# Kernel tuning notes

Hardware: AMD Instinct MI355X
Metric: run time of the kernel (lower is better)

Reference implementation:

```python
import jax, jax.numpy as jnp
import numpy as np


def setup_inputs() -> dict:
    key = jax.random.key(0)
    k1, k2, k3, k4 = jax.random.split(key, 4)
    B, S, IN, OUT, ORG = 8, 4096, 1536, 3072, 4
    fan_in_std = (1.0 / IN) ** 0.5
    x = jax.random.normal(k1, (B, S, IN), dtype=jnp.float32)
    weight = jax.random.normal(k2, (ORG, IN, OUT), dtype=jnp.float32) * fan_in_std
    bias = jax.random.normal(k3, (ORG, OUT), dtype=jnp.float32) * 0.01
    organism_index = jax.random.randint(k4, (B,), 0, ORG, dtype=jnp.int64)
    return {"x": x, "organism_index": organism_index, "weight": weight, "bias": bias}


def reference(x, organism_index, weight, bias):
    # Gather per-sample weight [B, IN, OUT] and bias [B, OUT]
    w = weight[organism_index].astype(x.dtype)          # [B, IN, OUT]
    b = bias[organism_index].astype(x.dtype)            # [B, OUT]
    # x: [B, S, IN] -> [B, S, OUT]; bias broadcast over inner dims
    out = jnp.einsum('bsi,bij->bsj', x, w) + b[:, None, :]
    return out
```

## Files before the change

kernel.cpp:

```cpp
#include <hip/hip_runtime.h>
#include <hip/hip_bf16.h>
#include <stdint.h>

typedef __attribute__((ext_vector_type(4))) float f32x4;
typedef __attribute__((ext_vector_type(8))) short short8;

#define DIM_S 4096
#define DIM_IN 1536
#define DIM_OUT 3072
#define NB 8
#define NORG 4

#define XB_ELEMS (NB * DIM_S * DIM_IN)
#define WT_ELEMS (NORG * DIM_OUT * DIM_IN)
#define WS_NEED ((size_t)(XB_ELEMS + WT_ELEMS) * 2)

__device__ __forceinline__ unsigned short f2bf(float f) {
    union { __hip_bfloat16 h; unsigned short u; } c;
    c.h = __float2bfloat16(f);
    return c.u;
}

__device__ __forceinline__ void gload16(const void* g, void* l) {
    __builtin_amdgcn_global_load_lds(
        (const __attribute__((address_space(1))) unsigned int*)g,
        (__attribute__((address_space(3))) unsigned int*)l, 16, 0, 0);
}

__global__ __launch_bounds__(256) void cvt_x(const float* __restrict__ x,
                                             unsigned short* __restrict__ xb) {
    const int nchunk = XB_ELEMS / 8;
    for (int c = blockIdx.x * 256 + threadIdx.x; c < nchunk; c += gridDim.x * 256) {
        const float4 v0 = *reinterpret_cast<const float4*>(x + (size_t)c * 8);
        const float4 v1 = *reinterpret_cast<const float4*>(x + (size_t)c * 8 + 4);
        union { unsigned short u[8]; short8 v; } p;
        p.u[0] = f2bf(v0.x); p.u[1] = f2bf(v0.y); p.u[2] = f2bf(v0.z); p.u[3] = f2bf(v0.w);
        p.u[4] = f2bf(v1.x); p.u[5] = f2bf(v1.y); p.u[6] = f2bf(v1.z); p.u[7] = f2bf(v1.w);
        *reinterpret_cast<short8*>(xb + (size_t)c * 8) = p.v;
    }
}

__global__ __launch_bounds__(256) void cvt_wt(const float* __restrict__ w,
                                              unsigned short* __restrict__ wt) {
    __shared__ unsigned short T[64][68];
    const int bid = blockIdx.x;
    const int org = bid / (24 * 48);
    const int rem = bid % (24 * 48);
    const int k0 = (rem / 48) * 64;
    const int n0 = (rem % 48) * 64;
    const float* __restrict__ wp = w + (size_t)org * DIM_IN * DIM_OUT;
    unsigned short* __restrict__ op = wt + (size_t)org * DIM_OUT * DIM_IN;
    const int t = threadIdx.x;
    #pragma unroll
    for (int i = 0; i < 4; ++i) {
        const int c = t + 256 * i;
        const int kk = c >> 4, nq = (c & 15) * 4;
        const float4 v = *reinterpret_cast<const float4*>(
            wp + (size_t)(k0 + kk) * DIM_OUT + n0 + nq);
        ushort4 pv;
        pv.x = f2bf(v.x); pv.y = f2bf(v.y); pv.z = f2bf(v.z); pv.w = f2bf(v.w);
        *reinterpret_cast<ushort4*>(&T[kk][nq]) = pv;
    }
    __syncthreads();
    #pragma unroll
    for (int i = 0; i < 2; ++i) {
        const int c = t + 256 * i;
        const int n = c >> 3, k8 = (c & 7) * 8;
        union { unsigned short u[8]; short8 v; } p;
        #pragma unroll
        for (int j = 0; j < 8; ++j) p.u[j] = T[k8 + j][n];
        *reinterpret_cast<short8*>(op + (size_t)(n0 + n) * DIM_IN + k0 + k8) = p.v;
    }
}

__global__ __launch_bounds__(512, 2) void mol_gemm_8p(
    const unsigned short* __restrict__ xb, const int* __restrict__ orgidx,
    const unsigned short* __restrict__ wt, const float* __restrict__ bias,
    float* __restrict__ out)
{
    __shared__ __align__(16) unsigned short LDS[2][4][8192];

    const int tid  = threadIdx.x;
    const int lane = tid & 63;
    const int wave = tid >> 6;
    const int wr = wave >> 2;
    const int wc = wave & 3;
    const int l15 = lane & 15;
    const int q16 = lane >> 4;

    const int bid = blockIdx.x;
    const int id  = (bid & 7) * 192 + (bid >> 3);
    const int row0 = (id / 12) * 256;
    const int col0 = (id % 12) * 256;
    const int batch = row0 >> 12;
    const int org   = orgidx[batch];

    const unsigned short* __restrict__ Abase = xb + (size_t)row0 * DIM_IN;
    const unsigned short* __restrict__ Bbase =
        wt + (size_t)org * DIM_OUT * DIM_IN + (size_t)col0 * DIM_IN;

    const int rA = tid >> 2;
    const int qs = ((tid & 3) ^ (((tid >> 5) & 1) << 1)) * 8;
    const unsigned short* pA0 = Abase + (size_t)rA * DIM_IN + qs;
    const unsigned short* pA1 = Abase + (size_t)(128 + rA) * DIM_IN + qs;
    const unsigned short* pB0 = Bbase + (size_t)rA * DIM_IN + qs;
    const unsigned short* pB1 = Bbase + (size_t)(128 + rA) * DIM_IN + qs;

    const int d0 = wave * 512;
    const int d1 = 4096 + wave * 512;

    const int swb = ((l15 >> 3) & 1) << 1;
    const int offA0 = ((wr * 128 + l15) * 32 + ((q16 ^ swb) << 3)) * 2;
    const int offB0 = ((wc * 64  + l15) * 32 + ((q16 ^ swb) << 3)) * 2;

    f32x4 acc[8][4] = {};
    short8 af4[4], bfr[4];

#define STG(buf, slot, p0, p1, kofs) do {                      \
        gload16((p0) + (kofs), &LDS[buf][slot][d0]);           \
        gload16((p1) + (kofs), &LDS[buf][slot][d1]);           \
    } while (0)

#define RD_A4(buf, kk, mih) do {                                            \
        const char* bA_ = (const char*)(&LDS[buf][kk][0]) + offA0           \
                          + 4096 * (mih);                                   \
        _Pragma("unroll")                                                   \
        for (int i_ = 0; i_ < 4; ++i_)                                      \
            af4[i_] = *reinterpret_cast<const short8*>(bA_ + 1024 * i_);    \
    } while (0)

#define RD_B4(buf, kk) do {                                                 \
        const char* bB_ = (const char*)(&LDS[buf][2 + (kk)][0]) + offB0;    \
        _Pragma("unroll")                                                   \
        for (int i_ = 0; i_ < 4; ++i_)                                      \
            bfr[i_] = *reinterpret_cast<const short8*>(bB_ + 1024 * i_);    \
    } while (0)

#define MM(mih) do {                                                        \
        __builtin_amdgcn_s_setprio(1);                                      \
        _Pragma("unroll")                                                   \
        for (int i_ = 0; i_ < 4; ++i_) {                                    \
            _Pragma("unroll")                                               \
            for (int n_ = 0; n_ < 4; ++n_)                                  \
                acc[(mih)*4 + i_][n_] =                                     \
                    __builtin_amdgcn_mfma_f32_16x16x32_bf16(                \
                        af4[i_], bfr[n_], acc[(mih)*4 + i_][n_], 0, 0, 0);  \
        }                                                                   \
        __builtin_amdgcn_s_setprio(0);                                      \
    } while (0)

#define BAR  do { __builtin_amdgcn_s_barrier();                             \
                  asm volatile("" ::: "memory"); } while (0)
#define SB0  __builtin_amdgcn_sched_barrier(0)
#define WAIT8 asm volatile("s_waitcnt vmcnt(8)" ::: "memory")

    STG(0, 0, pA0, pA1, 0);
    STG(0, 2, pB0, pB1, 0);
    STG(0, 1, pA0, pA1, 32);
    STG(0, 3, pB0, pB1, 32);
    STG(1, 0, pA0, pA1, 64);
    STG(1, 2, pB0, pB1, 64);
    WAIT8;
    BAR;

    int kA = 96, kB = 96;

#define PHASE(buf, kk, mih, sbuf, sslot, pp0, pp1, kref, wait8) do {        \
        RD_A4(buf, kk, mih);                                                \
        if ((mih) == 0) RD_B4(buf, kk);                                     \
        STG(sbuf, sslot, pp0, pp1, kref);                                   \
        if (kref < 1504) kref += 32;                                        \
        BAR; SB0;                                                           \
        MM(mih);                                                            \
        if (wait8) WAIT8;                                                   \
        BAR;                                                                \
    } while (0)

#define TILE(buf, obuf) do {                                                \
        PHASE(buf, 0, 0, obuf, 1, pA0, pA1, kA, 0);                         \
        PHASE(buf, 0, 1, obuf, 3, pB0, pB1, kB, 1);                         \
        PHASE(buf, 1, 0, buf,  0, pA0, pA1, kA, 0);                         \
        PHASE(buf, 1, 1, buf,  2, pB0, pB1, kB, 1);                         \
    } while (0)

    #pragma unroll 1
    for (int i = 0; i < 12; ++i) {
        TILE(0, 1);
        TILE(1, 0);
    }

    const float* __restrict__ bptr = bias + (size_t)org * DIM_OUT;
    const int crow = q16 * 4;
    const int ccol = l15;
    #pragma unroll
    for (int ni = 0; ni < 4; ++ni) {
        const int gc = col0 + wc * 64 + ni * 16 + ccol;
        const float bv = bptr[gc];
        #pragma unroll
        for (int mi = 0; mi < 8; ++mi) {
            const int gr = row0 + wr * 128 + mi * 16 + crow;
            #pragma unroll
            for (int r = 0; r < 4; ++r)
                out[(size_t)(gr + r) * DIM_OUT + gc] = acc[mi][ni][r] + bv;
        }
    }
#undef STG
#undef RD_A4
#undef RD_B4
#undef MM
#undef BAR
#undef SB0
#undef WAIT8
#undef PHASE
#undef TILE
}

#define BM 128
#define BN 128
#define BK 32
#define LDK 40
union BF8 { unsigned short u[8]; short8 v; };

__global__ __launch_bounds__(256) void mol_gemm_fb(
    const float* __restrict__ x, const int* __restrict__ orgidx,
    const float* __restrict__ weight, const float* __restrict__ bias,
    float* __restrict__ out)
{
    __shared__ __align__(16) unsigned short Alds[2][BM][LDK];
    __shared__ __align__(16) unsigned short Blds[2][BN][LDK];

    const int tid  = threadIdx.x;
    const int lane = tid & 63;
    const int wave = tid >> 6;
    const int wr = wave >> 1, wc = wave & 1;

    const int bid = blockIdx.x;
    const int id  = (bid & 7) * 768 + (bid >> 3);
    const int row0 = (id / 24) * BM;
    const int col0 = (id % 24) * BN;

    const int batch = row0 / DIM_S;
    const int org   = orgidx[batch];
    const float* __restrict__ W = weight + (size_t)org * DIM_IN * DIM_OUT;

    f32x4 acc[4][4] = {};
    const int ar  = tid >> 2;
    const int ak8 = (tid & 3) * 8;
    const int bn  = tid & 127;
    const int bg0 = tid >> 7;
    const float* __restrict__ xbase = x + (size_t)row0 * DIM_IN;
    const float* __restrict__ wbase = W + col0 + bn;

    auto stage = [&](int buf, int k0) {
        #pragma unroll
        for (int i = 0; i < 2; ++i) {
            const int r = ar + 64 * i;
            const float* xp = xbase + (size_t)r * DIM_IN + k0 + ak8;
            const float4 v0 = *reinterpret_cast<const float4*>(xp);
            const float4 v1 = *reinterpret_cast<const float4*>(xp + 4);
            BF8 p;
            p.u[0] = f2bf(v0.x); p.u[1] = f2bf(v0.y);
            p.u[2] = f2bf(v0.z); p.u[3] = f2bf(v0.w);
            p.u[4] = f2bf(v1.x); p.u[5] = f2bf(v1.y);
            p.u[6] = f2bf(v1.z); p.u[7] = f2bf(v1.w);
            *reinterpret_cast<short8*>(&Alds[buf][r][ak8]) = p.v;
        }
        #pragma unroll
        for (int j = 0; j < 2; ++j) {
            const int g = bg0 + 2 * j;
            const float* wp = wbase + (size_t)(k0 + 8 * g) * DIM_OUT;
            BF8 p;
            #pragma unroll
            for (int r = 0; r < 8; ++r) p.u[r] = f2bf(wp[(size_t)r * DIM_OUT]);
            *reinterpret_cast<short8*>(&Blds[buf][bn][8 * g]) = p.v;
        }
    };

    stage(0, 0);
    const int nk = DIM_IN / BK;
    const int kq = (lane >> 4) * 8;
    const int lr = lane & 15;

    for (int t = 0; t < nk; ++t) {
        __syncthreads();
        const int cur = t & 1;
        if (t + 1 < nk) stage(cur ^ 1, (t + 1) * BK);
        short8 a[4], b[4];
        #pragma unroll
        for (int mi = 0; mi < 4; ++mi)
            a[mi] = *reinterpret_cast<const short8*>(&Alds[cur][wr * 64 + mi * 16 + lr][kq]);
        #pragma unroll
        for (int ni = 0; ni < 4; ++ni)
            b[ni] = *reinterpret_cast<const short8*>(&Blds[cur][wc * 64 + ni * 16 + lr][kq]);
        #pragma unroll
        for (int mi = 0; mi < 4; ++mi)
            #pragma unroll
            for (int ni = 0; ni < 4; ++ni)
                acc[mi][ni] = __builtin_amdgcn_mfma_f32_16x16x32_bf16(
                    a[mi], b[ni], acc[mi][ni], 0, 0, 0);
    }

    const float* __restrict__ bptr = bias + (size_t)org * DIM_OUT;
    const int crow = (lane >> 4) * 4;
    const int ccol = lane & 15;
    #pragma unroll
    for (int ni = 0; ni < 4; ++ni) {
        const int gc = col0 + wc * 64 + ni * 16 + ccol;
        const float bv = bptr[gc];
        #pragma unroll
        for (int mi = 0; mi < 4; ++mi) {
            const int gr = row0 + wr * 64 + mi * 16 + crow;
            #pragma unroll
            for (int r = 0; r < 4; ++r)
                out[(size_t)(gr + r) * DIM_OUT + gc] = acc[mi][ni][r] + bv;
        }
    }
}

extern "C" void kernel_launch(void* const* d_in, const int* in_sizes, int n_in,
                              void* d_out, int out_size, void* d_ws, size_t ws_size,
                              hipStream_t stream)
{
    const float* x      = (const float*)d_in[0];
    const int*   orgidx = (const int*)d_in[1];
    const float* weight = (const float*)d_in[2];
    const float* bias   = (const float*)d_in[3];
    float* out = (float*)d_out;

    if (ws_size >= WS_NEED) {
        unsigned short* xbp = (unsigned short*)d_ws;
        unsigned short* wtp = xbp + XB_ELEMS;
        cvt_x<<<dim3(2048), dim3(256), 0, stream>>>(x, xbp);
        cvt_wt<<<dim3(NORG * 24 * 48), dim3(256), 0, stream>>>(weight, wtp);
        mol_gemm_8p<<<dim3(1536), dim3(512), 0, stream>>>(xbp, orgidx, wtp, bias, out);
    } else {
        mol_gemm_fb<<<dim3(6144), dim3(256), 0, stream>>>(x, orgidx, weight, bias, out);
    }
}
```

Measured before the change: 435.3 us.

## Double-buffer MFMA register fragments to overlap LDS reads with matrix math

Restructures the main GEMM loop so A/B fragments are read from LDS into a second register set while MFMAs run on the first, and removes the sched_barrier and one of the two barriers per phase. The waitcnt is changed from vmcnt(8) to vmcnt(4) to match the new staging order. The aim is to hide LDS read latency behind matrix work and cut synchronisation. In exchange it uses more VGPRs and relies on a delicate buffer-slot ordering, so any race or occupancy loss could offset the gain.

Result: no change. 429.0 us (-1.4%).

```diff
diff --git a/kernel.cpp b/kernel.cpp
--- a/kernel.cpp
+++ b/kernel.cpp
@@ -114,29 +114,29 @@
     const int offB0 = ((wc * 64  + l15) * 32 + ((q16 ^ swb) << 3)) * 2;
 
     f32x4 acc[8][4] = {};
-    short8 af4[4], bfr[4];
+    short8 af[2][4], bfr[2][4];
 
 #define STG(buf, slot, p0, p1, kofs) do {                      \
         gload16((p0) + (kofs), &LDS[buf][slot][d0]);           \
         gload16((p1) + (kofs), &LDS[buf][slot][d1]);           \
     } while (0)
 
-#define RD_A4(buf, kk, mih) do {                                            \
-        const char* bA_ = (const char*)(&LDS[buf][kk][0]) + offA0           \
+#define RD_A4(dst, buf, kk, mih) do {                                       \
+        const char* pA_ = (const char*)(&LDS[buf][kk][0]) + offA0           \
                           + 4096 * (mih);                                   \
         _Pragma("unroll")                                                   \
         for (int i_ = 0; i_ < 4; ++i_)                                      \
-            af4[i_] = *reinterpret_cast<const short8*>(bA_ + 1024 * i_);    \
+            af[dst][i_] = *reinterpret_cast<const short8*>(pA_ + 1024*i_);  \
     } while (0)
 
-#define RD_B4(buf, kk) do {                                                 \
-        const char* bB_ = (const char*)(&LDS[buf][2 + (kk)][0]) + offB0;    \
+#define RD_B4(dst, buf, kk) do {                                            \
+        const char* pB_ = (const char*)(&LDS[buf][2 + (kk)][0]) + offB0;    \
         _Pragma("unroll")                                                   \
         for (int i_ = 0; i_ < 4; ++i_)                                      \
-            bfr[i_] = *reinterpret_cast<const short8*>(bB_ + 1024 * i_);    \
+            bfr[dst][i_] = *reinterpret_cast<const short8*>(pB_ + 1024*i_); \
     } while (0)
 
-#define MM(mih) do {                                                        \
+#define MM(ca, cb, mih) do {                                                \
         __builtin_amdgcn_s_setprio(1);                                      \
         _Pragma("unroll")                                                   \
         for (int i_ = 0; i_ < 4; ++i_) {                                    \
@@ -144,15 +144,17 @@
             for (int n_ = 0; n_ < 4; ++n_)                                  \
                 acc[(mih)*4 + i_][n_] =                                     \
                     __builtin_amdgcn_mfma_f32_16x16x32_bf16(                \
-                        af4[i_], bfr[n_], acc[(mih)*4 + i_][n_], 0, 0, 0);  \
+                        af[ca][i_], bfr[cb][n_],                            \
+                        acc[(mih)*4 + i_][n_], 0, 0, 0);                    \
         }                                                                   \
         __builtin_amdgcn_s_setprio(0);                                      \
     } while (0)
 
 #define BAR  do { __builtin_amdgcn_s_barrier();                             \
                   asm volatile("" ::: "memory"); } while (0)
-#define SB0  __builtin_amdgcn_sched_barrier(0)
+#define WAIT4 asm volatile("s_waitcnt vmcnt(4)" ::: "memory")
 #define WAIT8 asm volatile("s_waitcnt vmcnt(8)" ::: "memory")
+#define KADV(k) do { if ((k) < 1504) (k) += 32; } while (0)
 
     STG(0, 0, pA0, pA1, 0);
     STG(0, 2, pB0, pB1, 0);
@@ -162,31 +164,33 @@
     STG(1, 2, pB0, pB1, 64);
     WAIT8;
     BAR;
+    RD_A4(0, 0, 0, 0);
+    RD_B4(0, 0, 0);
 
     int kA = 96, kB = 96;
 
-#define PHASE(buf, kk, mih, sbuf, sslot, pp0, pp1, kref, wait8) do {        \
-        RD_A4(buf, kk, mih);                                                \
-        if ((mih) == 0) RD_B4(buf, kk);                                     \
-        STG(sbuf, sslot, pp0, pp1, kref);                                   \
-        if (kref < 1504) kref += 32;                                        \
-        BAR; SB0;                                                           \
-        MM(mih);                                                            \
-        if (wait8) WAIT8;                                                   \
-        BAR;                                                                \
-    } while (0)
-
-#define TILE(buf, obuf) do {                                                \
-        PHASE(buf, 0, 0, obuf, 1, pA0, pA1, kA, 0);                         \
-        PHASE(buf, 0, 1, obuf, 3, pB0, pB1, kB, 1);                         \
-        PHASE(buf, 1, 0, buf,  0, pA0, pA1, kA, 0);                         \
-        PHASE(buf, 1, 1, buf,  2, pB0, pB1, kB, 1);                         \
-    } while (0)
+#define TILE2() do {                                                        \
+   STG(1,1,pA0,pA1,kA); KADV(kA); RD_A4(1, 0,0,1);                    \
+         MM(0,0,0);                 BAR;                                    \
+   STG(1,3,pB0,pB1,kB); KADV(kB); RD_A4(0, 0,1,0); RD_B4(1, 0,1);    \
+         MM(1,0,1);          WAIT4; BAR;                                    \
+   STG(0,0,pA0,pA1,kA); KADV(kA); RD_A4(1, 0,1,1);                    \
+         MM(0,1,0);                 BAR;                                    \
+   STG(0,2,pB0,pB1,kB); KADV(kB); RD_A4(0, 1,0,0); RD_B4(0, 1,0);    \
+         MM(1,1,1);          WAIT4; BAR;                                    \
+   STG(0,1,pA0,pA1,kA); KADV(kA); RD_A4(1, 1,0,1);                    \
+         MM(0,0,0);                 BAR;                                    \
+   STG(0,3,pB0,pB1,kB); KADV(kB); RD_A4(0, 1,1,0); RD_B4(1, 1,1);    \
+         MM(1,0,1);          WAIT4; BAR;                                    \
+   STG(1,0,pA0,pA1,kA); KADV(kA); RD_A4(1, 1,1,1);                    \
+         MM(0,1,0);                 BAR;                                    \
+   STG(1,2,pB0,pB1,kB); KADV(kB); RD_A4(0, 0,0,0); RD_B4(0, 0,0);    \
+         MM(1,1,1);          WAIT4; BAR;                                    \
+} while (0)
 
     #pragma unroll 1
     for (int i = 0; i < 12; ++i) {
-        TILE(0, 1);
-        TILE(1, 0);
+        TILE2();
     }
 
     const float* __restrict__ bptr = bias + (size_t)org * DIM_OUT;
@@ -209,10 +213,10 @@
 #undef RD_B4
 #undef MM
 #undef BAR
-#undef SB0
+#undef WAIT4
 #undef WAIT8
-#undef PHASE
-#undef TILE
+#undef KADV
+#undef TILE2
 }
 
 #define BM 128
```

## Replace 8-wave 256x256 GEMM with 4-wave 256x128 triple-buffered pipeline

Applied to the files above, without the earlier changes.

The main GEMM kernel moves from 512 threads on 256x256 tiles with a double-buffered two-half phase schedule to 256 threads on 256x128 tiles. It uses a three-stage LDS ring with one barrier per K-step, and global loads for the next stage are issued between the MFMA halves. This is meant to cut barrier count and improve latency hiding while keeping two blocks per CU. In exchange, the smaller N tile means A is reloaded twice as often, so global and L2 traffic per FLOP goes up, and the grid doubles to 3072 blocks.

After: 455.5 us. +4.6%, slower.

```diff
diff --git a/kernel.cpp b/kernel.cpp
--- a/kernel.cpp
+++ b/kernel.cpp
@@ -73,27 +73,26 @@
     }
 }
 
-__global__ __launch_bounds__(512, 2) void mol_gemm_8p(
+__global__ __launch_bounds__(256, 2) void mol_gemm_3b(
     const unsigned short* __restrict__ xb, const int* __restrict__ orgidx,
     const unsigned short* __restrict__ wt, const float* __restrict__ bias,
     float* __restrict__ out)
 {
-    __shared__ __align__(16) unsigned short LDS[2][4][8192];
+    __shared__ __align__(16) unsigned short LDS[3][12288];
 
     const int tid  = threadIdx.x;
     const int lane = tid & 63;
     const int wave = tid >> 6;
-    const int wr = wave >> 2;
-    const int wc = wave & 3;
+    const int wr = wave >> 1;
+    const int wc = wave & 1;
     const int l15 = lane & 15;
     const int q16 = lane >> 4;
 
     const int bid = blockIdx.x;
-    const int id  = (bid & 7) * 192 + (bid >> 3);
-    const int row0 = (id / 12) * 256;
-    const int col0 = (id % 12) * 256;
-    const int batch = row0 >> 12;
-    const int org   = orgidx[batch];
+    const int id  = (bid & 7) * 384 + (bid >> 3);
+    const int row0 = (id / 24) * 256;
+    const int col0 = (id % 24) * 128;
+    const int org  = orgidx[row0 >> 12];
 
     const unsigned short* __restrict__ Abase = xb + (size_t)row0 * DIM_IN;
     const unsigned short* __restrict__ Bbase =
@@ -101,39 +100,45 @@
 
     const int rA = tid >> 2;
     const int qs = ((tid & 3) ^ (((tid >> 5) & 1) << 1)) * 8;
-    const unsigned short* pA0 = Abase + (size_t)rA * DIM_IN + qs;
-    const unsigned short* pA1 = Abase + (size_t)(128 + rA) * DIM_IN + qs;
-    const unsigned short* pB0 = Bbase + (size_t)rA * DIM_IN + qs;
-    const unsigned short* pB1 = Bbase + (size_t)(128 + rA) * DIM_IN + qs;
-
-    const int d0 = wave * 512;
-    const int d1 = 4096 + wave * 512;
+    const unsigned short* pa0 = Abase + (size_t)(rA      ) * DIM_IN + qs;
+    const unsigned short* pa1 = Abase + (size_t)(rA +  64) * DIM_IN + qs;
+    const unsigned short* pa2 = Abase + (size_t)(rA + 128) * DIM_IN + qs;
+    const unsigned short* pa3 = Abase + (size_t)(rA + 192) * DIM_IN + qs;
+    const unsigned short* pb0 = Bbase + (size_t)(rA      ) * DIM_IN + qs;
+    const unsigned short* pb1 = Bbase + (size_t)(rA +  64) * DIM_IN + qs;
 
     const int swb = ((l15 >> 3) & 1) << 1;
-    const int offA0 = ((wr * 128 + l15) * 32 + ((q16 ^ swb) << 3)) * 2;
-    const int offB0 = ((wc * 64  + l15) * 32 + ((q16 ^ swb) << 3)) * 2;
+    const int lof = l15 * 64 + ((q16 ^ swb) << 4);
 
     f32x4 acc[8][4] = {};
     short8 af4[4], bfr[4];
 
-#define STG(buf, slot, p0, p1, kofs) do {                      \
-        gload16((p0) + (kofs), &LDS[buf][slot][d0]);           \
-        gload16((p1) + (kofs), &LDS[buf][slot][d1]);           \
-    } while (0)
-
-#define RD_A4(buf, kk, mih) do {                                            \
-        const char* bA_ = (const char*)(&LDS[buf][kk][0]) + offA0           \
-                          + 4096 * (mih);                                   \
+#define STG_A(bs, k) do {                                                   \
+        gload16(pa0 + (k), &LDS[bs][          wave * 512]);                 \
+        gload16(pa1 + (k), &LDS[bs][2048 +    wave * 512]);                 \
+        gload16(pa2 + (k), &LDS[bs][4096 +    wave * 512]);                 \
+        gload16(pa3 + (k), &LDS[bs][6144 +    wave * 512]);                 \
+    } while (0)
+
+#define STG_B(bs, k) do {                                                   \
+        gload16(pb0 + (k), &LDS[bs][8192 +         wave * 512]);            \
+        gload16(pb1 + (k), &LDS[bs][8192 + 2048 + wave * 512]);             \
+    } while (0)
+
+#define RD_A4(b, mih) do {                                                  \
+        const char* pA_ = (const char*)(&LDS[b][0])                         \
+                          + (wr * 8 + (mih) * 4) * 1024 + lof;              \
         _Pragma("unroll")                                                   \
         for (int i_ = 0; i_ < 4; ++i_)                                      \
-            af4[i_] = *reinterpret_cast<const short8*>(bA_ + 1024 * i_);    \
-    } while (0)
-
-#define RD_B4(buf, kk) do {                                                 \
-        const char* bB_ = (const char*)(&LDS[buf][2 + (kk)][0]) + offB0;    \
+            af4[i_] = *reinterpret_cast<const short8*>(pA_ + 1024 * i_);    \
+    } while (0)
+
+#define RD_B4(b) do {                                                       \
+        const char* pB_ = (const char*)(&LDS[b][0]) + 16384                 \
+                          + wc * 4096 + lof;                                \
         _Pragma("unroll")                                                   \
         for (int i_ = 0; i_ < 4; ++i_)                                      \
-            bfr[i_] = *reinterpret_cast<const short8*>(bB_ + 1024 * i_);    \
+            bfr[i_] = *reinterpret_cast<const short8*>(pB_ + 1024 * i_);    \
     } while (0)
 
 #define MM(mih) do {                                                        \
@@ -149,44 +154,28 @@
         __builtin_amdgcn_s_setprio(0);                                      \
     } while (0)
 
-#define BAR  do { __builtin_amdgcn_s_barrier();                             \
-                  asm volatile("" ::: "memory"); } while (0)
-#define SB0  __builtin_amdgcn_sched_barrier(0)
-#define WAIT8 asm volatile("s_waitcnt vmcnt(8)" ::: "memory")
-
-    STG(0, 0, pA0, pA1, 0);
-    STG(0, 2, pB0, pB1, 0);
-    STG(0, 1, pA0, pA1, 32);
-    STG(0, 3, pB0, pB1, 32);
-    STG(1, 0, pA0, pA1, 64);
-    STG(1, 2, pB0, pB1, 64);
-    WAIT8;
+#define BAR   asm volatile("s_barrier" ::: "memory")
+#define WAIT6 asm volatile("s_waitcnt vmcnt(6)" ::: "memory")
+
+    STG_A(0, 0);  STG_B(0, 0);
+    STG_A(1, 32); STG_B(1, 32);
+    WAIT6;
     BAR;
-
-    int kA = 96, kB = 96;
-
-#define PHASE(buf, kk, mih, sbuf, sslot, pp0, pp1, kref, wait8) do {        \
-        RD_A4(buf, kk, mih);                                                \
-        if ((mih) == 0) RD_B4(buf, kk);                                     \
-        STG(sbuf, sslot, pp0, pp1, kref);                                   \
-        if (kref < 1504) kref += 32;                                        \
-        BAR; SB0;                                                           \
-        MM(mih);                                                            \
-        if (wait8) WAIT8;                                                   \
-        BAR;                                                                \
-    } while (0)
-
-#define TILE(buf, obuf) do {                                                \
-        PHASE(buf, 0, 0, obuf, 1, pA0, pA1, kA, 0);                         \
-        PHASE(buf, 0, 1, obuf, 3, pB0, pB1, kB, 1);                         \
-        PHASE(buf, 1, 0, buf,  0, pA0, pA1, kA, 0);                         \
-        PHASE(buf, 1, 1, buf,  2, pB0, pB1, kB, 1);                         \
+    int kS = 64;
+
+#define TILE(b, bs) do {                                                    \
+        STG_A(bs, kS);                                                      \
+        RD_B4(b); RD_A4(b, 0); MM(0);                                       \
+        STG_B(bs, kS); if (kS < 1504) kS += 32;                             \
+        RD_A4(b, 1); MM(1);                                                 \
+        WAIT6; BAR;                                                         \
     } while (0)
 
     #pragma unroll 1
-    for (int i = 0; i < 12; ++i) {
-        TILE(0, 1);
+    for (int i = 0; i < 16; ++i) {
+        TILE(0, 2);
         TILE(1, 0);
+        TILE(2, 1);
     }
 
     const float* __restrict__ bptr = bias + (size_t)org * DIM_OUT;
@@ -204,14 +193,13 @@
                 out[(size_t)(gr + r) * DIM_OUT + gc] = acc[mi][ni][r] + bv;
         }
     }
-#undef STG
+#undef STG_A
+#undef STG_B
 #undef RD_A4
 #undef RD_B4
 #undef MM
 #undef BAR
-#undef SB0
-#undef WAIT8
-#undef PHASE
+#undef WAIT6
 #undef TILE
 }
 
@@ -332,7 +320,7 @@
         unsigned short* wtp = xbp + XB_ELEMS;
         cvt_x<<<dim3(2048), dim3(256), 0, stream>>>(x, xbp);
         cvt_wt<<<dim3(NORG * 24 * 48), dim3(256), 0, stream>>>(weight, wtp);
-        mol_gemm_8p<<<dim3(1536), dim3(512), 0, stream>>>(xbp, orgidx, wtp, bias, out);
+        mol_gemm_3b<<<dim3(3072), dim3(256), 0, stream>>>(xbp, orgidx, wtp, bias, out);
     } else {
         mol_gemm_fb<<<dim3(6144), dim3(256), 0, stream>>>(x, orgidx, weight, bias, out);
     }
```
